# Optimization experiments

Measured on AMD Instinct MI355X. Metric: run time of the kernel, lower is better.

The kernel has to match this reference:

```python
import jax, jax.numpy as jnp
import numpy as np

N = 50000      # nodes
E = 800000     # edges
F_IN = 128     # num_node_features
H = 128        # hidden_channels
C = 10         # num_classes
G = 512        # graphs in batch


def setup_inputs() -> dict:
    key = jax.random.key(0)
    ks = jax.random.split(key, 8)
    x = jax.random.normal(ks[0], (N, F_IN), dtype=jnp.float32)
    edge_index = jax.random.randint(ks[1], (2, E), 0, N, dtype=jnp.int64)
    batch = jnp.sort(jax.random.randint(ks[2], (N,), 0, G, dtype=jnp.int64))
    s = 1.0 / np.sqrt(F_IN)
    W1 = jax.random.normal(ks[3], (F_IN, H), dtype=jnp.float32) * s
    b1 = jnp.zeros((H,), dtype=jnp.float32)
    W2 = jax.random.normal(ks[4], (H, H), dtype=jnp.float32) * s
    b2 = jnp.zeros((H,), dtype=jnp.float32)
    Wl = jax.random.normal(ks[5], (H, C), dtype=jnp.float32) * s
    bl = jnp.zeros((C,), dtype=jnp.float32)
    return {"x": x, "edge_index": edge_index, "batch": batch,
            "W1": W1, "b1": b1, "W2": W2, "b2": b2, "Wl": Wl, "bl": bl}


def _gcn_conv(h, src, dst, deg_inv_sqrt, W, b):
    # PyG GCNConv: x @ W, then symmetric-normalized scatter-add with self-loops.
    h = h @ W                                   # [N, H]
    norm = deg_inv_sqrt[src] * deg_inv_sqrt[dst]  # [E]
    msg = h[src] * norm[:, None]                # gather + scale, [E, H]
    out = jax.ops.segment_sum(msg, dst, num_segments=N)
    # self-loop contribution (deg already includes +1):
    out = out + h * (deg_inv_sqrt * deg_inv_sqrt)[:, None]
    return out + b


def reference(x, edge_index, batch, W1, b1, W2, b2, Wl, bl):
    src, dst = edge_index[0], edge_index[1]
    # degree on destination nodes, +1 for self-loops (PyG default)
    deg = jax.ops.segment_sum(jnp.ones((E,), x.dtype), dst, num_segments=N) + 1.0
    deg_inv_sqrt = jax.lax.rsqrt(deg)

    h = jax.nn.relu(_gcn_conv(x, src, dst, deg_inv_sqrt, W1, b1))
    h = jax.nn.relu(_gcn_conv(h, src, dst, deg_inv_sqrt, W2, b2))

    # global mean pool over graphs
    sums = jax.ops.segment_sum(h, batch, num_segments=G)          # [G, H]
    counts = jax.ops.segment_sum(jnp.ones((N,), h.dtype), batch, num_segments=G)
    pooled = sums / jnp.clip(counts, 1.0)[:, None]
    # dropout p=0.5 is identity in eval mode
    return pooled @ Wl + bl
```

## Files before the change

### kernel.cpp

```cpp
#include <hip/hip_runtime.h>
#include <hip/hip_bf16.h>
#include <hip/hip_fp16.h>

typedef unsigned short ushort_t;
typedef unsigned int uint32;
typedef __attribute__((ext_vector_type(8))) _Float16 half8;
typedef __attribute__((ext_vector_type(4))) float floatx4;

#define KMAX 64
#define BSHIFT 6
#define BCAP2 1280
#define MAXBUK 800

__device__ __forceinline__ uint32 pack2h(float a, float b) {
    return (uint32)__half_as_ushort(__float2half(a)) |
           ((uint32)__half_as_ushort(__float2half(b)) << 16);
}
__device__ __forceinline__ float2 unpack2h(uint32 q) {
    __half2 hh = *reinterpret_cast<__half2*>(&q);
    return __half22float2(hh);
}

__global__ __launch_bounds__(256) void binmm_k(
    const int* __restrict__ ei, int* __restrict__ bcur,
    uint32* __restrict__ binned, int E, int nbuk, int BB,
    const float* __restrict__ x, const float* __restrict__ W,
    uint32* __restrict__ t2, int N,
    const int* __restrict__ batch, int* __restrict__ gstart, int G) {
    __shared__ __align__(16) char smem[34816];
    int tid = threadIdx.x;
    if (blockIdx.x < BB) {
        int* hist = (int*)smem;
        int* lbase = hist + MAXBUK;
        for (int i = tid; i < nbuk; i += 256) hist[i] = 0;
        __syncthreads();
        int base = blockIdx.x * 4096;
        uint32 ed[16];
        int bk[16];
        #pragma unroll
        for (int i = 0; i < 16; ++i) {
            int e = base + i * 256 + tid;
            if (e < E) {
                int s = ei[e], d = ei[E + e];
                ed[i] = (uint32)s | ((uint32)d << 16);
                bk[i] = d >> BSHIFT;
                atomicAdd(&hist[bk[i]], 1);
            } else bk[i] = -1;
        }
        __syncthreads();
        for (int i = tid; i < nbuk; i += 256) lbase[i] = atomicAdd(&bcur[i], hist[i]);
        __syncthreads();
        for (int i = tid; i < nbuk; i += 256) hist[i] = 0;
        __syncthreads();
        #pragma unroll
        for (int i = 0; i < 16; ++i) {
            if (bk[i] >= 0) {
                int p = atomicAdd(&hist[bk[i]], 1);
                int idx = lbase[bk[i]] + p;
                if (idx < BCAP2) binned[(size_t)bk[i] * BCAP2 + idx] = ed[i];
            }
        }
    } else {
        int bid = blockIdx.x - BB;
        int i0 = bid * 256 + tid;
        if (i0 <= G) {
            int lo = 0, hi = N;
            while (lo < hi) {
                int mid = (lo + hi) >> 1;
                if (batch[mid] < i0) lo = mid + 1; else hi = mid;
            }
            gstart[i0] = lo;
        }
        ushort_t (*Wh)[136] = (ushort_t(*)[136])smem;
        for (int i = tid; i < 128 * 128; i += 256) {
            int k = i >> 7, c = i & 127;
            Wh[c][k] = __half_as_ushort(__float2half(W[i]));
        }
        __syncthreads();

        int wave = tid >> 6, lane = tid & 63;
        int row0 = bid * 64 + wave * 16;
        int m = lane & 15;
        int arow = row0 + m;
        int koff = (lane >> 4) * 8;
        bool valid = arow < N;

        floatx4 acc[8];
        #pragma unroll
        for (int nt = 0; nt < 8; ++nt) acc[nt] = (floatx4){0.f, 0.f, 0.f, 0.f};

        for (int kk = 0; kk < 4; ++kk) {
            int k = kk * 32 + koff;
            union { uint32 u[4]; half8 h; } av;
            av.u[0] = av.u[1] = av.u[2] = av.u[3] = 0;
            if (valid) {
                const float* p = x + (size_t)arow * 128 + k;
                floatx4 f0 = *(const floatx4*)p;
                floatx4 f1 = *(const floatx4*)(p + 4);
                av.u[0] = pack2h(f0[0], f0[1]);
                av.u[1] = pack2h(f0[2], f0[3]);
                av.u[2] = pack2h(f1[0], f1[1]);
                av.u[3] = pack2h(f1[2], f1[3]);
            }
            half8 af = av.h;
            #pragma unroll
            for (int nt = 0; nt < 8; ++nt) {
                int col = nt * 16 + m;
                half8 bf = *(const half8*)(&Wh[col][k]);
                acc[nt] = __builtin_amdgcn_mfma_f32_16x16x32_f16(af, bf, acc[nt], 0, 0, 0);
            }
        }
        int r0 = (lane >> 4) * 4;
        #pragma unroll
        for (int nt = 0; nt < 4; ++nt) {
            int c = nt * 16 + m;
            #pragma unroll
            for (int r = 0; r < 4; ++r) {
                int row = row0 + r0 + r;
                if (row < N)
                    t2[(size_t)row * 64 + c] = pack2h(acc[nt][r], acc[nt + 4][r]);
            }
        }
    }
}

__global__ __launch_bounds__(256) void fill4_k(const uint32* __restrict__ binned,
                                               const int* __restrict__ bcur,
                                               int* __restrict__ cnt,
                                               ushort_t* __restrict__ slot,
                                               uint32* __restrict__ t2, int N) {
    __shared__ ushort_t ls[64 * KMAX];
    __shared__ int lc[64];
    __shared__ float dsf[64];
    int b = blockIdx.x;
    int tid = threadIdx.x;
    if (tid < 64) lc[tid] = 0;
    __syncthreads();
    int ne = bcur[b];
    if (ne > BCAP2) ne = BCAP2;
    const uint32* src = binned + (size_t)b * BCAP2;
    int nbase = b << BSHIFT;
    for (int i = tid; i < ne; i += 256) {
        uint32 ed = src[i];
        int s = (int)(ed & 0xFFFFu);
        int d = (int)(ed >> 16) - nbase;
        int p = atomicAdd(&lc[d], 1);
        if (p < KMAX) ls[(d << 6) + p] = (ushort_t)s;
    }
    __syncthreads();
    int nn = N - nbase;
    if (nn > 64) nn = 64;
    if (tid < 64) {
        if (tid < nn) cnt[nbase + tid] = lc[tid];
        dsf[tid] = rsqrtf((float)lc[tid] + 1.0f);
    }
    uint4* gs = (uint4*)(slot + ((size_t)nbase << 6));
    const uint4* lsv = (const uint4*)ls;
    int totalv = nn * 8;
    for (int i = tid; i < totalv; i += 256) gs[i] = lsv[i];
    __syncthreads();
    int tot = nn * 64;
    for (int i = tid; i < tot; i += 256) {
        int r = i >> 6, c = i & 63;
        size_t idx = ((size_t)(nbase + r) << 6) + c;
        float ds = dsf[r];
        float2 f = unpack2h(t2[idx]);
        t2[idx] = pack2h(f.x * ds, f.y * ds);
    }
}

__global__ __launch_bounds__(256) void gemm2_k(const uint32* __restrict__ Av,
                                               const float* __restrict__ W,
                                               uint32* __restrict__ t2, int N,
                                               const int* __restrict__ cnt) {
    int tid = threadIdx.x;
    __shared__ ushort_t Wh[128][136];
    for (int i = tid; i < 128 * 128; i += 256) {
        int k = i >> 7, c = i & 127;
        Wh[c][k] = __half_as_ushort(__float2half(W[i]));
    }
    __syncthreads();

    int wave = tid >> 6, lane = tid & 63;
    int row0 = blockIdx.x * 64 + wave * 16;
    int m = lane & 15;
    int arow = row0 + m;
    int koff = (lane >> 4) * 8;
    bool valid = arow < N;

    floatx4 acc[8];
    #pragma unroll
    for (int nt = 0; nt < 8; ++nt) acc[nt] = (floatx4){0.f, 0.f, 0.f, 0.f};

    for (int kk = 0; kk < 4; ++kk) {
        int k = kk * 32 + koff;
        union { uint32 u[4]; half8 h; } av;
        av.u[0] = av.u[1] = av.u[2] = av.u[3] = 0;
        if (valid) {
            const uint32* hp = Av + (size_t)arow * 64 + (k & 63);
            uint4 w0 = *(const uint4*)hp;
            uint4 w1 = *(const uint4*)(hp + 4);
            uint32 ws[8] = {w0.x, w0.y, w0.z, w0.w, w1.x, w1.y, w1.z, w1.w};
            if (k >= 64) {
                #pragma unroll
                for (int j = 0; j < 4; ++j)
                    av.u[j] = (ws[2 * j] >> 16) | (ws[2 * j + 1] & 0xFFFF0000u);
            } else {
                #pragma unroll
                for (int j = 0; j < 4; ++j)
                    av.u[j] = (ws[2 * j] & 0xFFFFu) | (ws[2 * j + 1] << 16);
            }
        }
        half8 af = av.h;
        #pragma unroll
        for (int nt = 0; nt < 8; ++nt) {
            int col = nt * 16 + m;
            half8 bf = *(const half8*)(&Wh[col][k]);
            acc[nt] = __builtin_amdgcn_mfma_f32_16x16x32_f16(af, bf, acc[nt], 0, 0, 0);
        }
    }

    int r0 = (lane >> 4) * 4;
    float dsc[4];
    #pragma unroll
    for (int r = 0; r < 4; ++r) {
        int row = row0 + r0 + r;
        dsc[r] = (row < N) ? rsqrtf((float)cnt[row] + 1.0f) : 0.f;
    }
    #pragma unroll
    for (int nt = 0; nt < 4; ++nt) {
        int c = nt * 16 + m;
        #pragma unroll
        for (int r = 0; r < 4; ++r) {
            int row = row0 + r0 + r;
            if (row < N)
                t2[(size_t)row * 64 + c] =
                    pack2h(acc[nt][r] * dsc[r], acc[nt + 4][r] * dsc[r]);
        }
    }
}

__global__ __launch_bounds__(256) void agg_k(const uint32* __restrict__ t2,
                                             const int* __restrict__ cnt,
                                             const ushort_t* __restrict__ slot,
                                             const float* __restrict__ bias,
                                             uint32* __restrict__ outp, int N) {
    int wave = threadIdx.x >> 6, lane = threadIdx.x & 63;
    int n = blockIdx.x * 4 + wave;
    if (n >= N) return;
    int deg = cnt[n];
    float d = rsqrtf((float)deg + 1.0f);
    if (deg > KMAX) deg = KMAX;
    float2 self = unpack2h(t2[(size_t)n * 64 + lane]);
    float acc0 = self.x;
    float acc1 = self.y;
    const ushort_t* sl = slot + (size_t)n * KMAX;
    int i = 0;
    for (; i + 16 <= deg; i += 16) {
        uint4 qa = *(const uint4*)(sl + i);
        uint4 qb = *(const uint4*)(sl + i + 8);
        uint32 sw[8] = {qa.x, qa.y, qa.z, qa.w, qb.x, qb.y, qb.z, qb.w};
        int s[16];
        #pragma unroll
        for (int u = 0; u < 8; ++u) {
            s[2 * u] = (int)(sw[u] & 0xFFFFu);
            s[2 * u + 1] = (int)(sw[u] >> 16);
        }
        float2 f[16];
        #pragma unroll
        for (int u = 0; u < 16; ++u)
            f[u] = unpack2h(t2[(size_t)s[u] * 64 + lane]);
        #pragma unroll
        for (int u = 0; u < 16; ++u) {
            acc0 += f[u].x;
            acc1 += f[u].y;
        }
    }
    for (; i + 4 <= deg; i += 4) {
        uint2 qa = *(const uint2*)(sl + i);
        int s[4] = {(int)(qa.x & 0xFFFFu), (int)(qa.x >> 16),
                    (int)(qa.y & 0xFFFFu), (int)(qa.y >> 16)};
        float2 f[4];
        #pragma unroll
        for (int u = 0; u < 4; ++u)
            f[u] = unpack2h(t2[(size_t)s[u] * 64 + lane]);
        #pragma unroll
        for (int u = 0; u < 4; ++u) {
            acc0 += f[u].x;
            acc1 += f[u].y;
        }
    }
    for (; i < deg; ++i) {
        float2 f = unpack2h(t2[(size_t)sl[i] * 64 + lane]);
        acc0 += f.x;
        acc1 += f.y;
    }
    acc0 = fmaxf(acc0 * d + bias[lane], 0.f);
    acc1 = fmaxf(acc1 * d + bias[lane + 64], 0.f);
    outp[(size_t)n * 64 + lane] = pack2h(acc0, acc1);
}

__global__ __launch_bounds__(256) void pool2_k(const uint32* __restrict__ h2,
                                               const int* __restrict__ gstart,
                                               const float* __restrict__ Wl,
                                               const float* __restrict__ bl,
                                               float* __restrict__ out, int C) {
    __shared__ float s0[256];
    __shared__ float s1[256];
    __shared__ float m[128];
    int g = blockIdx.x;
    int s = gstart[g], e = gstart[g + 1];
    int w = threadIdx.x & 63;
    int sub = threadIdx.x >> 6;
    float a0 = 0.f, a1 = 0.f;
    for (int n = s + sub; n < e; n += 4) {
        float2 f = unpack2h(h2[(size_t)n * 64 + w]);
        a0 += f.x;
        a1 += f.y;
    }
    s0[threadIdx.x] = a0;
    s1[threadIdx.x] = a1;
    __syncthreads();
    if (threadIdx.x < 64) {
        float inv = 1.f / fmaxf((float)(e - s), 1.f);
        m[w]      = (s0[w] + s0[w + 64] + s0[w + 128] + s0[w + 192]) * inv;
        m[w + 64] = (s1[w] + s1[w + 64] + s1[w + 128] + s1[w + 192]) * inv;
    }
    __syncthreads();
    if (threadIdx.x < C) {
        float sum = bl[threadIdx.x];
        #pragma unroll 4
        for (int jj = 0; jj < 128; ++jj)
            sum += m[jj] * Wl[jj * C + threadIdx.x];
        out[g * C + threadIdx.x] = sum;
    }
}

extern "C" void kernel_launch(void* const* d_in, const int* in_sizes, int n_in,
                              void* d_out, int out_size, void* d_ws, size_t ws_size,
                              hipStream_t stream) {
    const float* x   = (const float*)d_in[0];
    const int* ei    = (const int*)d_in[1];
    const int* batch = (const int*)d_in[2];
    const float* W1  = (const float*)d_in[3];
    const float* b1  = (const float*)d_in[4];
    const float* W2  = (const float*)d_in[5];
    const float* b2  = (const float*)d_in[6];
    const float* Wl  = (const float*)d_in[7];
    const float* bl  = (const float*)d_in[8];
    float* out = (float*)d_out;

    int N = in_sizes[2];
    int E = in_sizes[1] / 2;
    int C = in_sizes[8];
    int G = out_size / C;
    int nbuk = (N + 63) >> BSHIFT;

    char* w = (char*)d_ws;
    auto alloc = [&](size_t bytes) -> void* {
        void* p = (void*)w;
        w += (bytes + 255) & ~(size_t)255;
        return p;
    };
    int* bcur       = (int*)alloc((size_t)nbuk * 4);
    int* cnt        = (int*)alloc((size_t)N * 4);
    int* gstart     = (int*)alloc((size_t)(G + 1) * 4);
    ushort_t* slot  = (ushort_t*)alloc((size_t)nbuk * 64 * KMAX * 2);
    uint32* binned  = (uint32*)alloc((size_t)nbuk * BCAP2 * 4);
    uint32* t2      = (uint32*)alloc((size_t)N * 64 * 4);
    uint32* h1      = (uint32*)alloc((size_t)N * 64 * 4);
    uint32* h2      = (uint32*)alloc((size_t)N * 64 * 4);

    hipMemsetAsync(bcur, 0, (size_t)nbuk * 4, stream);

    int GB = (N + 63) / 64;
    int AB = (N + 3) / 4;
    int BB = (E + 4095) / 4096;

    binmm_k<<<BB + GB, 256, 0, stream>>>(ei, bcur, binned, E, nbuk, BB,
                                         x, W1, t2, N, batch, gstart, G);
    fill4_k<<<nbuk, 256, 0, stream>>>(binned, bcur, cnt, slot, t2, N);
    agg_k<<<AB, 256, 0, stream>>>(t2, cnt, slot, b1, h1, N);
    gemm2_k<<<GB, 256, 0, stream>>>(h1, W2, t2, N, cnt);
    agg_k<<<AB, 256, 0, stream>>>(t2, cnt, slot, b2, h2, N);
    pool2_k<<<G, 256, 0, stream>>>(h2, gstart, Wl, bl, out, C);
}
```

Before: 209.8 us.

## Fuse layer-1 aggregation into GEMM2 and second aggregation into pooling

The first neighbor aggregation is merged into the second-layer GEMM kernel: each block aggregates its 64 rows into shared memory, then runs the MFMA GEMM on that tile. This removes the h1 round trip through global memory and one launch. The second aggregation now adds its results straight into per-graph sums with atomics, which removes the h2 buffer and the pooling read pass. The trade-off is that only 64-node blocks are available for the latency-bound gather in the fused kernel, which lowers parallelism. The pooling path adds float atomic contention and a non-deterministic summation order.

```diff
diff --git a/kernel.cpp b/kernel.cpp
--- a/kernel.cpp
+++ b/kernel.cpp
@@ -11,6 +11,7 @@
 #define BSHIFT 6
 #define BCAP2 1280
 #define MAXBUK 800
+#define ASTRIDE 68
 
 __device__ __forceinline__ uint32 pack2h(float a, float b) {
     return (uint32)__half_as_ushort(__float2half(a)) |
@@ -169,24 +170,83 @@
     }
 }
 
-__global__ __launch_bounds__(256) void gemm2_k(const uint32* __restrict__ Av,
+__global__ __launch_bounds__(256) void aggmm_k(const uint32* __restrict__ t2,
+                                               const int* __restrict__ cnt,
+                                               const ushort_t* __restrict__ slot,
+                                               const float* __restrict__ bias,
                                                const float* __restrict__ W,
-                                               uint32* __restrict__ t2, int N,
-                                               const int* __restrict__ cnt) {
+                                               uint32* __restrict__ t2out, int N) {
+    __shared__ ushort_t Wh[128][136];
+    __shared__ uint32 At[64 * ASTRIDE];
     int tid = threadIdx.x;
-    __shared__ ushort_t Wh[128][136];
     for (int i = tid; i < 128 * 128; i += 256) {
         int k = i >> 7, c = i & 127;
         Wh[c][k] = __half_as_ushort(__float2half(W[i]));
     }
+    int wave = tid >> 6, lane = tid & 63;
+    int nbase = blockIdx.x * 64;
+
+    for (int t = 0; t < 16; ++t) {
+        int n = nbase + wave * 16 + t;
+        float acc0 = 0.f, acc1 = 0.f;
+        if (n < N) {
+            int deg = cnt[n];
+            float d = rsqrtf((float)deg + 1.0f);
+            if (deg > KMAX) deg = KMAX;
+            float2 self = unpack2h(t2[(size_t)n * 64 + lane]);
+            acc0 = self.x;
+            acc1 = self.y;
+            const ushort_t* sl = slot + (size_t)n * KMAX;
+            int i = 0;
+            for (; i + 16 <= deg; i += 16) {
+                uint4 qa = *(const uint4*)(sl + i);
+                uint4 qb = *(const uint4*)(sl + i + 8);
+                uint32 sw[8] = {qa.x, qa.y, qa.z, qa.w, qb.x, qb.y, qb.z, qb.w};
+                int s[16];
+                #pragma unroll
+                for (int u = 0; u < 8; ++u) {
+                    s[2 * u] = (int)(sw[u] & 0xFFFFu);
+                    s[2 * u + 1] = (int)(sw[u] >> 16);
+                }
+                float2 f[16];
+                #pragma unroll
+                for (int u = 0; u < 16; ++u)
+                    f[u] = unpack2h(t2[(size_t)s[u] * 64 + lane]);
+                #pragma unroll
+                for (int u = 0; u < 16; ++u) {
+                    acc0 += f[u].x;
+                    acc1 += f[u].y;
+                }
+            }
+            for (; i + 4 <= deg; i += 4) {
+                uint2 qa = *(const uint2*)(sl + i);
+                int s[4] = {(int)(qa.x & 0xFFFFu), (int)(qa.x >> 16),
+                            (int)(qa.y & 0xFFFFu), (int)(qa.y >> 16)};
+                float2 f[4];
+                #pragma unroll
+                for (int u = 0; u < 4; ++u)
+                    f[u] = unpack2h(t2[(size_t)s[u] * 64 + lane]);
+                #pragma unroll
+                for (int u = 0; u < 4; ++u) {
+                    acc0 += f[u].x;
+                    acc1 += f[u].y;
+                }
+            }
+            for (; i < deg; ++i) {
+                float2 f = unpack2h(t2[(size_t)sl[i] * 64 + lane]);
+                acc0 += f.x;
+                acc1 += f.y;
+            }
+            acc0 = fmaxf(acc0 * d + bias[lane], 0.f);
+            acc1 = fmaxf(acc1 * d + bias[lane + 64], 0.f);
+        }
+        At[(wave * 16 + t) * ASTRIDE + lane] = pack2h(acc0, acc1);
+    }
     __syncthreads();
 
-    int wave = tid >> 6, lane = tid & 63;
-    int row0 = blockIdx.x * 64 + wave * 16;
     int m = lane & 15;
-    int arow = row0 + m;
     int koff = (lane >> 4) * 8;
-    bool valid = arow < N;
+    int lrow = wave * 16 + m;
 
     floatx4 acc[8];
     #pragma unroll
@@ -194,22 +254,19 @@
 
     for (int kk = 0; kk < 4; ++kk) {
         int k = kk * 32 + koff;
+        const uint32* hp = &At[lrow * ASTRIDE + (k & 63)];
+        uint4 w0 = *(const uint4*)hp;
+        uint4 w1 = *(const uint4*)(hp + 4);
+        uint32 ws[8] = {w0.x, w0.y, w0.z, w0.w, w1.x, w1.y, w1.z, w1.w};
         union { uint32 u[4]; half8 h; } av;
-        av.u[0] = av.u[1] = av.u[2] = av.u[3] = 0;
-        if (valid) {
-            const uint32* hp = Av + (size_t)arow * 64 + (k & 63);
-            uint4 w0 = *(const uint4*)hp;
-            uint4 w1 = *(const uint4*)(hp + 4);
-            uint32 ws[8] = {w0.x, w0.y, w0.z, w0.w, w1.x, w1.y, w1.z, w1.w};
-            if (k >= 64) {
-                #pragma unroll
-                for (int j = 0; j < 4; ++j)
-                    av.u[j] = (ws[2 * j] >> 16) | (ws[2 * j + 1] & 0xFFFF0000u);
-            } else {
-                #pragma unroll
-                for (int j = 0; j < 4; ++j)
-                    av.u[j] = (ws[2 * j] & 0xFFFFu) | (ws[2 * j + 1] << 16);
-            }
+        if (k >= 64) {
+            #pragma unroll
+            for (int j = 0; j < 4; ++j)
+                av.u[j] = (ws[2 * j] >> 16) | (ws[2 * j + 1] & 0xFFFF0000u);
+        } else {
+            #pragma unroll
+            for (int j = 0; j < 4; ++j)
+                av.u[j] = (ws[2 * j] & 0xFFFFu) | (ws[2 * j + 1] << 16);
         }
         half8 af = av.h;
         #pragma unroll
@@ -221,6 +278,7 @@
     }
 
     int r0 = (lane >> 4) * 4;
+    int row0 = nbase + wave * 16;
     float dsc[4];
     #pragma unroll
     for (int r = 0; r < 4; ++r) {
@@ -234,17 +292,18 @@
         for (int r = 0; r < 4; ++r) {
             int row = row0 + r0 + r;
             if (row < N)
-                t2[(size_t)row * 64 + c] =
+                t2out[(size_t)row * 64 + c] =
                     pack2h(acc[nt][r] * dsc[r], acc[nt + 4][r] * dsc[r]);
         }
     }
 }
 
-__global__ __launch_bounds__(256) void agg_k(const uint32* __restrict__ t2,
-                                             const int* __restrict__ cnt,
-                                             const ushort_t* __restrict__ slot,
-                                             const float* __restrict__ bias,
-                                             uint32* __restrict__ outp, int N) {
+__global__ __launch_bounds__(256) void aggpool_k(const uint32* __restrict__ t2,
+                                                 const int* __restrict__ cnt,
+                                                 const ushort_t* __restrict__ slot,
+                                                 const float* __restrict__ bias,
+                                                 const int* __restrict__ batch,
+                                                 float* __restrict__ gsum, int N) {
     int wave = threadIdx.x >> 6, lane = threadIdx.x & 63;
     int n = blockIdx.x * 4 + wave;
     if (n >= N) return;
@@ -297,35 +356,20 @@
     }
     acc0 = fmaxf(acc0 * d + bias[lane], 0.f);
     acc1 = fmaxf(acc1 * d + bias[lane + 64], 0.f);
-    outp[(size_t)n * 64 + lane] = pack2h(acc0, acc1);
-}
-
-__global__ __launch_bounds__(256) void pool2_k(const uint32* __restrict__ h2,
-                                               const int* __restrict__ gstart,
-                                               const float* __restrict__ Wl,
-                                               const float* __restrict__ bl,
-                                               float* __restrict__ out, int C) {
-    __shared__ float s0[256];
-    __shared__ float s1[256];
+    int g = batch[n];
+    atomicAdd(&gsum[(size_t)g * 128 + lane], acc0);
+    atomicAdd(&gsum[(size_t)g * 128 + 64 + lane], acc1);
+}
+
+__global__ __launch_bounds__(128) void poolfin_k(const float* __restrict__ gsum,
+                                                 const int* __restrict__ gstart,
+                                                 const float* __restrict__ Wl,
+                                                 const float* __restrict__ bl,
+                                                 float* __restrict__ out, int C) {
     __shared__ float m[128];
     int g = blockIdx.x;
-    int s = gstart[g], e = gstart[g + 1];
-    int w = threadIdx.x & 63;
-    int sub = threadIdx.x >> 6;
-    float a0 = 0.f, a1 = 0.f;
-    for (int n = s + sub; n < e; n += 4) {
-        float2 f = unpack2h(h2[(size_t)n * 64 + w]);
-        a0 += f.x;
-        a1 += f.y;
-    }
-    s0[threadIdx.x] = a0;
-    s1[threadIdx.x] = a1;
-    __syncthreads();
-    if (threadIdx.x < 64) {
-        float inv = 1.f / fmaxf((float)(e - s), 1.f);
-        m[w]      = (s0[w] + s0[w + 64] + s0[w + 128] + s0[w + 192]) * inv;
-        m[w + 64] = (s1[w] + s1[w + 64] + s1[w + 128] + s1[w + 192]) * inv;
-    }
+    float inv = 1.f / fmaxf((float)(gstart[g + 1] - gstart[g]), 1.f);
+    m[threadIdx.x] = gsum[(size_t)g * 128 + threadIdx.x] * inv;
     __syncthreads();
     if (threadIdx.x < C) {
         float sum = bl[threadIdx.x];
@@ -368,10 +412,11 @@
     ushort_t* slot  = (ushort_t*)alloc((size_t)nbuk * 64 * KMAX * 2);
     uint32* binned  = (uint32*)alloc((size_t)nbuk * BCAP2 * 4);
     uint32* t2      = (uint32*)alloc((size_t)N * 64 * 4);
-    uint32* h1      = (uint32*)alloc((size_t)N * 64 * 4);
-    uint32* h2      = (uint32*)alloc((size_t)N * 64 * 4);
+    uint32* t2b     = (uint32*)alloc((size_t)N * 64 * 4);
+    float* gsum     = (float*)alloc((size_t)G * 128 * 4);
 
     hipMemsetAsync(bcur, 0, (size_t)nbuk * 4, stream);
+    hipMemsetAsync(gsum, 0, (size_t)G * 128 * 4, stream);
 
     int GB = (N + 63) / 64;
     int AB = (N + 3) / 4;
@@ -380,8 +425,7 @@
     binmm_k<<<BB + GB, 256, 0, stream>>>(ei, bcur, binned, E, nbuk, BB,
                                          x, W1, t2, N, batch, gstart, G);
     fill4_k<<<nbuk, 256, 0, stream>>>(binned, bcur, cnt, slot, t2, N);
-    agg_k<<<AB, 256, 0, stream>>>(t2, cnt, slot, b1, h1, N);
-    gemm2_k<<<GB, 256, 0, stream>>>(h1, W2, t2, N, cnt);
-    agg_k<<<AB, 256, 0, stream>>>(t2, cnt, slot, b2, h2, N);
-    pool2_k<<<G, 256, 0, stream>>>(h2, gstart, Wl, bl, out, C);
-}
+    aggmm_k<<<GB, 256, 0, stream>>>(t2, cnt, slot, b1, W2, t2b, N);
+    aggpool_k<<<AB, 256, 0, stream>>>(t2b, cnt, slot, b2, batch, gsum, N);
+    poolfin_k<<<G, 128, 0, stream>>>(gsum, gstart, Wl, bl, out, C);
+}
```

New measurement: 262.2 us. 25.0% more time.

## Pad neighbor slots with zero row and fuse second aggregation with pooling

Applied to the files above, without the earlier changes.

Neighbor slot lists are pre-filled with a sentinel index N that points to a zero row appended to the feature buffers. This lets aggregation always gather in full rounds of 16 with no tail loops or branches. The second aggregation now atomically adds ReLU outputs into per-graph sums instead of writing h2, and a small finalize kernel does the mean and the linear layer. The cost is extra gathers of the zero row for low-degree nodes and atomic contention on per-graph sums, plus two extra memsets.

```diff
diff --git a/kernel.cpp b/kernel.cpp
--- a/kernel.cpp
+++ b/kernel.cpp
@@ -129,23 +129,26 @@
                                                int* __restrict__ cnt,
                                                ushort_t* __restrict__ slot,
                                                uint32* __restrict__ t2, int N) {
-    __shared__ ushort_t ls[64 * KMAX];
+    __shared__ uint32 ls[64 * KMAX / 2];
     __shared__ int lc[64];
     __shared__ float dsf[64];
     int b = blockIdx.x;
     int tid = threadIdx.x;
     if (tid < 64) lc[tid] = 0;
+    uint32 sv2 = (uint32)(ushort_t)N | ((uint32)(ushort_t)N << 16);
+    for (int i = tid; i < 64 * KMAX / 2; i += 256) ls[i] = sv2;
     __syncthreads();
     int ne = bcur[b];
     if (ne > BCAP2) ne = BCAP2;
     const uint32* src = binned + (size_t)b * BCAP2;
     int nbase = b << BSHIFT;
+    ushort_t* lsu = (ushort_t*)ls;
     for (int i = tid; i < ne; i += 256) {
         uint32 ed = src[i];
         int s = (int)(ed & 0xFFFFu);
         int d = (int)(ed >> 16) - nbase;
         int p = atomicAdd(&lc[d], 1);
-        if (p < KMAX) ls[(d << 6) + p] = (ushort_t)s;
+        if (p < KMAX) lsu[(d << 6) + p] = (ushort_t)s;
     }
     __syncthreads();
     int nn = N - nbase;
@@ -167,6 +170,52 @@
         float2 f = unpack2h(t2[idx]);
         t2[idx] = pack2h(f.x * ds, f.y * ds);
     }
+}
+
+__device__ __forceinline__ void gather16(const uint32* __restrict__ t2,
+                                         const ushort_t* __restrict__ sl,
+                                         int lane, float& acc0, float& acc1) {
+    uint4 qa = *(const uint4*)(sl);
+    uint4 qb = *(const uint4*)(sl + 8);
+    uint32 sw[8] = {qa.x, qa.y, qa.z, qa.w, qb.x, qb.y, qb.z, qb.w};
+    int s[16];
+    #pragma unroll
+    for (int u = 0; u < 8; ++u) {
+        s[2 * u] = (int)(sw[u] & 0xFFFFu);
+        s[2 * u + 1] = (int)(sw[u] >> 16);
+    }
+    float2 f[16];
+    #pragma unroll
+    for (int u = 0; u < 16; ++u)
+        f[u] = unpack2h(t2[(size_t)s[u] * 64 + lane]);
+    #pragma unroll
+    for (int u = 0; u < 16; ++u) {
+        acc0 += f[u].x;
+        acc1 += f[u].y;
+    }
+}
+
+__global__ __launch_bounds__(256) void agg_k(const uint32* __restrict__ t2,
+                                             const int* __restrict__ cnt,
+                                             const ushort_t* __restrict__ slot,
+                                             const float* __restrict__ bias,
+                                             uint32* __restrict__ outp, int N) {
+    int wave = threadIdx.x >> 6, lane = threadIdx.x & 63;
+    int n = blockIdx.x * 4 + wave;
+    if (n >= N) return;
+    int deg = cnt[n];
+    float d = rsqrtf((float)deg + 1.0f);
+    if (deg > KMAX) deg = KMAX;
+    float2 self = unpack2h(t2[(size_t)n * 64 + lane]);
+    float acc0 = self.x;
+    float acc1 = self.y;
+    const ushort_t* sl = slot + (size_t)n * KMAX;
+    int rounds = (deg + 15) >> 4;
+    for (int rr = 0; rr < rounds; ++rr)
+        gather16(t2, sl + rr * 16, lane, acc0, acc1);
+    acc0 = fmaxf(acc0 * d + bias[lane], 0.f);
+    acc1 = fmaxf(acc1 * d + bias[lane + 64], 0.f);
+    outp[(size_t)n * 64 + lane] = pack2h(acc0, acc1);
 }
 
 __global__ __launch_bounds__(256) void gemm2_k(const uint32* __restrict__ Av,
@@ -240,11 +289,12 @@
     }
 }
 
-__global__ __launch_bounds__(256) void agg_k(const uint32* __restrict__ t2,
-                                             const int* __restrict__ cnt,
-                                             const ushort_t* __restrict__ slot,
-                                             const float* __restrict__ bias,
-                                             uint32* __restrict__ outp, int N) {
+__global__ __launch_bounds__(256) void aggpool_k(const uint32* __restrict__ t2,
+                                                 const int* __restrict__ cnt,
+                                                 const ushort_t* __restrict__ slot,
+                                                 const float* __restrict__ bias,
+                                                 const int* __restrict__ batch,
+                                                 float* __restrict__ gsum, int N) {
     int wave = threadIdx.x >> 6, lane = threadIdx.x & 63;
     int n = blockIdx.x * 4 + wave;
     if (n >= N) return;
@@ -255,77 +305,25 @@
     float acc0 = self.x;
     float acc1 = self.y;
     const ushort_t* sl = slot + (size_t)n * KMAX;
-    int i = 0;
-    for (; i + 16 <= deg; i += 16) {
-        uint4 qa = *(const uint4*)(sl + i);
-        uint4 qb = *(const uint4*)(sl + i + 8);
-        uint32 sw[8] = {qa.x, qa.y, qa.z, qa.w, qb.x, qb.y, qb.z, qb.w};
-        int s[16];
-        #pragma unroll
-        for (int u = 0; u < 8; ++u) {
-            s[2 * u] = (int)(sw[u] & 0xFFFFu);
-            s[2 * u + 1] = (int)(sw[u] >> 16);
-        }
-        float2 f[16];
-        #pragma unroll
-        for (int u = 0; u < 16; ++u)
-            f[u] = unpack2h(t2[(size_t)s[u] * 64 + lane]);
-        #pragma unroll
-        for (int u = 0; u < 16; ++u) {
-            acc0 += f[u].x;
-            acc1 += f[u].y;
-        }
-    }
-    for (; i + 4 <= deg; i += 4) {
-        uint2 qa = *(const uint2*)(sl + i);
-        int s[4] = {(int)(qa.x & 0xFFFFu), (int)(qa.x >> 16),
-                    (int)(qa.y & 0xFFFFu), (int)(qa.y >> 16)};
-        float2 f[4];
-        #pragma unroll
-        for (int u = 0; u < 4; ++u)
-            f[u] = unpack2h(t2[(size_t)s[u] * 64 + lane]);
-        #pragma unroll
-        for (int u = 0; u < 4; ++u) {
-            acc0 += f[u].x;
-            acc1 += f[u].y;
-        }
-    }
-    for (; i < deg; ++i) {
-        float2 f = unpack2h(t2[(size_t)sl[i] * 64 + lane]);
-        acc0 += f.x;
-        acc1 += f.y;
-    }
+    int rounds = (deg + 15) >> 4;
+    for (int rr = 0; rr < rounds; ++rr)
+        gather16(t2, sl + rr * 16, lane, acc0, acc1);
     acc0 = fmaxf(acc0 * d + bias[lane], 0.f);
     acc1 = fmaxf(acc1 * d + bias[lane + 64], 0.f);
-    outp[(size_t)n * 64 + lane] = pack2h(acc0, acc1);
-}
-
-__global__ __launch_bounds__(256) void pool2_k(const uint32* __restrict__ h2,
-                                               const int* __restrict__ gstart,
-                                               const float* __restrict__ Wl,
-                                               const float* __restrict__ bl,
-                                               float* __restrict__ out, int C) {
-    __shared__ float s0[256];
-    __shared__ float s1[256];
+    int g = batch[n];
+    atomicAdd(&gsum[(size_t)g * 128 + lane], acc0);
+    atomicAdd(&gsum[(size_t)g * 128 + 64 + lane], acc1);
+}
+
+__global__ __launch_bounds__(128) void poolfin_k(const float* __restrict__ gsum,
+                                                 const int* __restrict__ gstart,
+                                                 const float* __restrict__ Wl,
+                                                 const float* __restrict__ bl,
+                                                 float* __restrict__ out, int C) {
     __shared__ float m[128];
     int g = blockIdx.x;
-    int s = gstart[g], e = gstart[g + 1];
-    int w = threadIdx.x & 63;
-    int sub = threadIdx.x >> 6;
-    float a0 = 0.f, a1 = 0.f;
-    for (int n = s + sub; n < e; n += 4) {
-        float2 f = unpack2h(h2[(size_t)n * 64 + w]);
-        a0 += f.x;
-        a1 += f.y;
-    }
-    s0[threadIdx.x] = a0;
-    s1[threadIdx.x] = a1;
-    __syncthreads();
-    if (threadIdx.x < 64) {
-        float inv = 1.f / fmaxf((float)(e - s), 1.f);
-        m[w]      = (s0[w] + s0[w + 64] + s0[w + 128] + s0[w + 192]) * inv;
-        m[w + 64] = (s1[w] + s1[w + 64] + s1[w + 128] + s1[w + 192]) * inv;
-    }
+    float inv = 1.f / fmaxf((float)(gstart[g + 1] - gstart[g]), 1.f);
+    m[threadIdx.x] = gsum[(size_t)g * 128 + threadIdx.x] * inv;
     __syncthreads();
     if (threadIdx.x < C) {
         float sum = bl[threadIdx.x];
@@ -367,11 +365,15 @@
     int* gstart     = (int*)alloc((size_t)(G + 1) * 4);
     ushort_t* slot  = (ushort_t*)alloc((size_t)nbuk * 64 * KMAX * 2);
     uint32* binned  = (uint32*)alloc((size_t)nbuk * BCAP2 * 4);
-    uint32* t2      = (uint32*)alloc((size_t)N * 64 * 4);
+    uint32* t2      = (uint32*)alloc((size_t)(N + 1) * 64 * 4);
     uint32* h1      = (uint32*)alloc((size_t)N * 64 * 4);
-    uint32* h2      = (uint32*)alloc((size_t)N * 64 * 4);
+    uint32* t2b     = (uint32*)alloc((size_t)(N + 1) * 64 * 4);
+    float* gsum     = (float*)alloc((size_t)G * 128 * 4);
 
     hipMemsetAsync(bcur, 0, (size_t)nbuk * 4, stream);
+    hipMemsetAsync(gsum, 0, (size_t)G * 128 * 4, stream);
+    hipMemsetAsync(t2 + (size_t)N * 64, 0, 256, stream);
+    hipMemsetAsync(t2b + (size_t)N * 64, 0, 256, stream);
 
     int GB = (N + 63) / 64;
     int AB = (N + 3) / 4;
@@ -381,7 +383,7 @@
                                          x, W1, t2, N, batch, gstart, G);
     fill4_k<<<nbuk, 256, 0, stream>>>(binned, bcur, cnt, slot, t2, N);
     agg_k<<<AB, 256, 0, stream>>>(t2, cnt, slot, b1, h1, N);
-    gemm2_k<<<GB, 256, 0, stream>>>(h1, W2, t2, N, cnt);
-    agg_k<<<AB, 256, 0, stream>>>(t2, cnt, slot, b2, h2, N);
-    pool2_k<<<G, 256, 0, stream>>>(h2, gstart, Wl, bl, out, C);
-}
+    gemm2_k<<<GB, 256, 0, stream>>>(h1, W2, t2b, N, cnt);
+    aggpool_k<<<AB, 256, 0, stream>>>(t2b, cnt, slot, b2, batch, gsum, N);
+    poolfin_k<<<G, 128, 0, stream>>>(gsum, gstart, Wl, bl, out, C);
+}
```

Result: faster. 202.0 us (-3.7%).
